# Kernel tuning notes

Hardware: AMD Instinct MI355X
Metric: run time of the kernel (lower is better)

## Reference

```python
import jax, jax.numpy as jnp
import numpy as np

B = 262144          # batch
D = 128             # in_dim == out_dim
BS = 16             # block size
K = 8               # number of blocks
RANK = 4            # low-rank blocks' rank
DENSE = np.array([0, 3, 6])   # block ids with mode 'dense'
DIAG = np.array([1, 4, 7])    # block ids with mode 'diagonal'
LR = np.array([2, 5])         # block ids with mode 'lowrank'
EPS = 1e-8


def setup_inputs() -> dict:
    key = jax.random.key(0)
    k1, k2, k3, k4, k5 = jax.random.split(key, 5)
    x = jax.random.normal(k1, (B, D), dtype=jnp.float32)
    # dense blocks: torch init is identity (d_in==d_out); add noise so math is non-trivial
    W_dense = jnp.eye(BS, dtype=jnp.float32)[None] + 0.1 * jax.random.normal(k2, (len(DENSE), BS, BS), dtype=jnp.float32)
    # diagonal blocks: torch init is ones; perturb slightly
    s_diag = 1.0 + 0.1 * jax.random.normal(k3, (len(DIAG), BS), dtype=jnp.float32)
    # lowrank blocks: xavier-uniform-like scale
    lim = float(np.sqrt(6.0 / (BS + RANK)))
    U = jax.random.uniform(k4, (len(LR), BS, RANK), dtype=jnp.float32, minval=-lim, maxval=lim)
    V = jax.random.uniform(k5, (len(LR), BS, RANK), dtype=jnp.float32, minval=-lim, maxval=lim)
    return {"x": x, "W_dense": W_dense, "s_diag": s_diag, "U": U, "V": V}


def reference(x, W_dense, s_diag, U, V):
    # blocks are contiguous [16*j, 16*(j+1)), so gather == reshape to [B, K, BS]
    x3 = x.reshape(B, K, BS)
    # dense blocks: torch Linear y = x @ W.T, W is [d_out, d_in]
    yd = jnp.einsum('bkd,kod->bko', x3[:, DENSE], W_dense)
    # diagonal blocks: elementwise scale
    yg = x3[:, DIAG] * s_diag
    # lowrank blocks: x @ V @ U.T
    yl = jnp.einsum('bkr,kor->bko', jnp.einsum('bkd,kdr->bkr', x3[:, LR], V), U)
    y = jnp.zeros_like(x3).at[:, DENSE].set(yd).at[:, DIAG].set(yg).at[:, LR].set(yl)
    y = y.reshape(B, D)
    # l2 normalize (normalize=True)
    norm = jnp.linalg.norm(y, axis=-1, keepdims=True)
    return y / (norm + EPS)
```

## Files before the change

### kernel.cpp

```cpp
#include <hip/hip_runtime.h>

#define BATCH   262144
#define DDIM    128

__global__ __launch_bounds__(256, 4) void bdla_kernel(
    const float* __restrict__ x,
    const float* __restrict__ Wd,
    const float* __restrict__ sd,
    const float* __restrict__ U,
    const float* __restrict__ V,
    float* __restrict__ out)
{
    __shared__ float lds[1072];
    const int tid = threadIdx.x;
    for (int i = tid; i < 768; i += 256) lds[i] = Wd[i];
    if (tid < 48)  lds[768 + tid] = sd[tid];
    if (tid < 128) lds[816 + tid] = U[tid];
    if (tid < 128) lds[944 + tid] = V[tid];
    __syncthreads();

    const int lane   = tid & 63;
    const int lane32 = lane & 31;
    const int half   = lane >> 5;
    const int j      = lane32 >> 2;
    const int sub    = lane32 & 3;
    const int mode   = j % 3;
    const int k      = j / 3;

    float A[4][16];
    if (mode == 0) {
        const float* w = &lds[k * 256];
#pragma unroll
        for (int oo = 0; oo < 4; ++oo) {
            const int o = sub * 4 + oo;
#pragma unroll
            for (int m = 0; m < 4; ++m)
#pragma unroll
                for (int c = 0; c < 4; ++c)
                    A[oo][m * 4 + c] = w[o * 16 + ((sub ^ m) * 4 + c)];
        }
    } else if (mode == 1) {
        const float* s = &lds[768 + k * 16];
#pragma unroll
        for (int oo = 0; oo < 4; ++oo)
#pragma unroll
            for (int m = 0; m < 4; ++m)
#pragma unroll
                for (int c = 0; c < 4; ++c)
                    A[oo][m * 4 + c] = (m == 0 && c == oo) ? s[sub * 4 + oo] : 0.0f;
    } else {
        const float* u = &lds[816 + k * 64];
        const float* v = &lds[944 + k * 64];
#pragma unroll
        for (int oo = 0; oo < 4; ++oo) {
            const int o = sub * 4 + oo;
#pragma unroll
            for (int m = 0; m < 4; ++m)
#pragma unroll
                for (int c = 0; c < 4; ++c) {
                    const int d = (sub ^ m) * 4 + c;
                    float acc = 0.0f;
#pragma unroll
                    for (int r = 0; r < 4; ++r)
                        acc += u[o * 4 + r] * v[d * 4 + r];
                    A[oo][m * 4 + c] = acc;
                }
        }
    }

    const int wavesPerBlock = 256 / 64;
    const int gwave     = blockIdx.x * wavesPerBlock + (tid >> 6);
    const int rowStride = gridDim.x * wavesPerBlock * 2;

    int row = gwave * 2 + half;
    if (row >= BATCH) return;

    const float* xp = x + (size_t)row * DDIM + lane32 * 4;
    float4 xv = *(const float4*)xp;

    while (true) {
        const int nrow = row + rowStride;
        const bool has = (nrow < BATCH);
        float4 xn;
        if (has) xn = *(const float4*)(x + (size_t)nrow * DDIM + lane32 * 4);

        float g[16];
        g[0] = xv.x; g[1] = xv.y; g[2] = xv.z; g[3] = xv.w;
        g[4]  = __shfl_xor(xv.x, 1); g[5]  = __shfl_xor(xv.y, 1);
        g[6]  = __shfl_xor(xv.z, 1); g[7]  = __shfl_xor(xv.w, 1);
        g[8]  = __shfl_xor(xv.x, 2); g[9]  = __shfl_xor(xv.y, 2);
        g[10] = __shfl_xor(xv.z, 2); g[11] = __shfl_xor(xv.w, 2);
        g[12] = __shfl_xor(xv.x, 3); g[13] = __shfl_xor(xv.y, 3);
        g[14] = __shfl_xor(xv.z, 3); g[15] = __shfl_xor(xv.w, 3);

        float y0 = 0.f, y1 = 0.f, y2 = 0.f, y3 = 0.f;
#pragma unroll
        for (int t = 0; t < 16; ++t) {
            y0 = fmaf(A[0][t], g[t], y0);
            y1 = fmaf(A[1][t], g[t], y1);
            y2 = fmaf(A[2][t], g[t], y2);
            y3 = fmaf(A[3][t], g[t], y3);
        }

        float ss = y0 * y0 + y1 * y1 + y2 * y2 + y3 * y3;
        ss += __shfl_xor(ss, 1);
        ss += __shfl_xor(ss, 2);
        ss += __shfl_xor(ss, 4);
        ss += __shfl_xor(ss, 8);
        ss += __shfl_xor(ss, 16);
        const float inv = 1.0f / (sqrtf(ss) + 1e-8f);

        float4 yv;
        yv.x = y0 * inv; yv.y = y1 * inv; yv.z = y2 * inv; yv.w = y3 * inv;
        *(float4*)(out + (size_t)row * DDIM + lane32 * 4) = yv;

        if (!has) break;
        row = nrow;
        xv  = xn;
    }
}

extern "C" void kernel_launch(void* const* d_in, const int* in_sizes, int n_in,
                              void* d_out, int out_size, void* d_ws, size_t ws_size,
                              hipStream_t stream) {
    const float* x  = (const float*)d_in[0];
    const float* Wd = (const float*)d_in[1];
    const float* sd = (const float*)d_in[2];
    const float* U  = (const float*)d_in[3];
    const float* V  = (const float*)d_in[4];
    float* out = (float*)d_out;
    (void)in_sizes; (void)n_in; (void)out_size; (void)d_ws; (void)ws_size;

    dim3 grid(2048), block(256);
    hipLaunchKernelGGL(bdla_kernel, grid, block, 0, stream, x, Wd, sd, U, V, out);
}
```

Measured before the change: 264.5 us.

## Process two rows per half-wave with depth-2 prefetch and fixed unrolled loop

Each half-wave now handles two rows per iteration, and the grid-stride loop becomes a fully unrolled fixed-count loop that prefetches inputs two iterations ahead. The block-diagonal coefficient matrix is pinned in registers via empty asm constraints, and the occupancy hint is relaxed from 4 to 3 blocks. The aim is more outstanding memory requests per wave to better saturate HBM bandwidth. In exchange, register pressure rises, occupancy may fall, and the kernel now hardcodes the batch-to-grid mapping.

```diff
diff --git a/kernel.cpp b/kernel.cpp
--- a/kernel.cpp
+++ b/kernel.cpp
@@ -2,8 +2,10 @@
 
 #define BATCH   262144
 #define DDIM    128
+#define GRID    2048
+#define NITER   8
 
-__global__ __launch_bounds__(256, 4) void bdla_kernel(
+__global__ __launch_bounds__(256, 3) void bdla_kernel(
     const float* __restrict__ x,
     const float* __restrict__ Wd,
     const float* __restrict__ sd,
@@ -68,55 +70,76 @@
         }
     }
 
-    const int wavesPerBlock = 256 / 64;
-    const int gwave     = blockIdx.x * wavesPerBlock + (tid >> 6);
-    const int rowStride = gridDim.x * wavesPerBlock * 2;
+#pragma unroll
+    for (int oo = 0; oo < 4; ++oo)
+#pragma unroll
+        for (int t = 0; t < 16; ++t)
+            asm volatile("" : "+v"(A[oo][t]));
 
-    int row = gwave * 2 + half;
-    if (row >= BATCH) return;
+    const int gw = blockIdx.x * 4 + (tid >> 6);
+    const float* xbase = x   + (size_t)(gw * 4 + half) * DDIM + lane32 * 4;
+    float*       obase = out + (size_t)(gw * 4 + half) * DDIM + lane32 * 4;
+    const size_t istep = (size_t)(GRID * 4 * 4) * DDIM;
 
-    const float* xp = x + (size_t)row * DDIM + lane32 * 4;
-    float4 xv = *(const float4*)xp;
+    float4 a0 = *(const float4*)(xbase);
+    float4 b0 = *(const float4*)(xbase + 2 * DDIM);
+    float4 a1 = *(const float4*)(xbase + istep);
+    float4 b1 = *(const float4*)(xbase + istep + 2 * DDIM);
 
-    while (true) {
-        const int nrow = row + rowStride;
-        const bool has = (nrow < BATCH);
-        float4 xn;
-        if (has) xn = *(const float4*)(x + (size_t)nrow * DDIM + lane32 * 4);
+#pragma unroll
+    for (int it = 0; it < NITER; ++it) {
+        float4 a2, b2;
+        if (it + 2 < NITER) {
+            a2 = *(const float4*)(xbase + (size_t)(it + 2) * istep);
+            b2 = *(const float4*)(xbase + (size_t)(it + 2) * istep + 2 * DDIM);
+        }
 
-        float g[16];
-        g[0] = xv.x; g[1] = xv.y; g[2] = xv.z; g[3] = xv.w;
-        g[4]  = __shfl_xor(xv.x, 1); g[5]  = __shfl_xor(xv.y, 1);
-        g[6]  = __shfl_xor(xv.z, 1); g[7]  = __shfl_xor(xv.w, 1);
-        g[8]  = __shfl_xor(xv.x, 2); g[9]  = __shfl_xor(xv.y, 2);
-        g[10] = __shfl_xor(xv.z, 2); g[11] = __shfl_xor(xv.w, 2);
-        g[12] = __shfl_xor(xv.x, 3); g[13] = __shfl_xor(xv.y, 3);
-        g[14] = __shfl_xor(xv.z, 3); g[15] = __shfl_xor(xv.w, 3);
+        float ga[16], gb[16];
+        ga[0] = a0.x; ga[1] = a0.y; ga[2] = a0.z; ga[3] = a0.w;
+        gb[0] = b0.x; gb[1] = b0.y; gb[2] = b0.z; gb[3] = b0.w;
+#pragma unroll
+        for (int m = 1; m < 4; ++m) {
+            ga[m * 4 + 0] = __shfl_xor(a0.x, m);
+            ga[m * 4 + 1] = __shfl_xor(a0.y, m);
+            ga[m * 4 + 2] = __shfl_xor(a0.z, m);
+            ga[m * 4 + 3] = __shfl_xor(a0.w, m);
+            gb[m * 4 + 0] = __shfl_xor(b0.x, m);
+            gb[m * 4 + 1] = __shfl_xor(b0.y, m);
+            gb[m * 4 + 2] = __shfl_xor(b0.z, m);
+            gb[m * 4 + 3] = __shfl_xor(b0.w, m);
+        }
 
-        float y0 = 0.f, y1 = 0.f, y2 = 0.f, y3 = 0.f;
+        float ya0 = 0.f, ya1 = 0.f, ya2 = 0.f, ya3 = 0.f;
+        float yb0 = 0.f, yb1 = 0.f, yb2 = 0.f, yb3 = 0.f;
 #pragma unroll
         for (int t = 0; t < 16; ++t) {
-            y0 = fmaf(A[0][t], g[t], y0);
-            y1 = fmaf(A[1][t], g[t], y1);
-            y2 = fmaf(A[2][t], g[t], y2);
-            y3 = fmaf(A[3][t], g[t], y3);
+            ya0 = fmaf(A[0][t], ga[t], ya0);
+            ya1 = fmaf(A[1][t], ga[t], ya1);
+            ya2 = fmaf(A[2][t], ga[t], ya2);
+            ya3 = fmaf(A[3][t], ga[t], ya3);
+            yb0 = fmaf(A[0][t], gb[t], yb0);
+            yb1 = fmaf(A[1][t], gb[t], yb1);
+            yb2 = fmaf(A[2][t], gb[t], yb2);
+            yb3 = fmaf(A[3][t], gb[t], yb3);
         }
 
-        float ss = y0 * y0 + y1 * y1 + y2 * y2 + y3 * y3;
-        ss += __shfl_xor(ss, 1);
-        ss += __shfl_xor(ss, 2);
-        ss += __shfl_xor(ss, 4);
-        ss += __shfl_xor(ss, 8);
-        ss += __shfl_xor(ss, 16);
-        const float inv = 1.0f / (sqrtf(ss) + 1e-8f);
+        float ssa = ya0 * ya0 + ya1 * ya1 + ya2 * ya2 + ya3 * ya3;
+        float ssb = yb0 * yb0 + yb1 * yb1 + yb2 * yb2 + yb3 * yb3;
+#pragma unroll
+        for (int m = 1; m < 32; m <<= 1) {
+            ssa += __shfl_xor(ssa, m);
+            ssb += __shfl_xor(ssb, m);
+        }
+        const float inva = 1.0f / (sqrtf(ssa) + 1e-8f);
+        const float invb = 1.0f / (sqrtf(ssb) + 1e-8f);
 
-        float4 yv;
-        yv.x = y0 * inv; yv.y = y1 * inv; yv.z = y2 * inv; yv.w = y3 * inv;
-        *(float4*)(out + (size_t)row * DDIM + lane32 * 4) = yv;
+        float4 yva, yvb;
+        yva.x = ya0 * inva; yva.y = ya1 * inva; yva.z = ya2 * inva; yva.w = ya3 * inva;
+        yvb.x = yb0 * invb; yvb.y = yb1 * invb; yvb.z = yb2 * invb; yvb.w = yb3 * invb;
+        *(float4*)(obase + (size_t)it * istep)            = yva;
+        *(float4*)(obase + (size_t)it * istep + 2 * DDIM) = yvb;
 
-        if (!has) break;
-        row = nrow;
-        xv  = xn;
+        a0 = a1; b0 = b1; a1 = a2; b1 = b2;
     }
 }
 
@@ -131,6 +154,6 @@
     float* out = (float*)d_out;
     (void)in_sizes; (void)n_in; (void)out_size; (void)d_ws; (void)ws_size;
 
-    dim3 grid(2048), block(256);
+    dim3 grid(GRID), block(256);
     hipLaunchKernelGGL(bdla_kernel, grid, block, 0, stream, x, Wd, sd, U, V, out);
 }
```

New measurement: 241.0 us. 8.9% less time.
